# Performance work log

Measured on AMD Instinct MI355X. Metric: run time of the kernel, lower is better.

## Reference

```python
import jax, jax.numpy as jnp
import numpy as np
from jax import lax

VOCAB, EMB, FILT, ATT, KW = 50000, 300, 400, 200, 3
B, N = 4096, 30

def setup_inputs() -> dict:
    key = jax.random.key(0)
    ks = jax.random.split(key, 7)
    encoded_title = jax.random.randint(ks[0], (B, N), 0, VOCAB)
    emb = jax.random.normal(ks[1], (VOCAB, EMB), dtype=jnp.float32) * 0.1
    conv_w = jax.random.normal(ks[2], (FILT, EMB, KW), dtype=jnp.float32) * (1.0 / np.sqrt(EMB * KW))
    conv_b = jnp.zeros((FILT,), dtype=jnp.float32)
    v = jax.random.normal(ks[3], (FILT, ATT), dtype=jnp.float32) * (1.0 / np.sqrt(FILT))
    vb = jnp.zeros((ATT,), dtype=jnp.float32)
    q = jax.random.normal(ks[4], (ATT, 1), dtype=jnp.float32) * (1.0 / np.sqrt(ATT))
    return {"encoded_title": encoded_title, "emb": emb, "conv_w": conv_w,
            "conv_b": conv_b, "v": v, "vb": vb, "q": q}

def reference(encoded_title, emb, conv_w, conv_b, v, vb, q):
    mask = (encoded_title != 0).astype(jnp.float32)          # [B, N]
    W = emb[encoded_title]                                    # [B, N, E]
    x = jnp.transpose(W, (0, 2, 1))                           # [B, E, N]
    C = lax.conv_general_dilated(x, conv_w, window_strides=(1,),
                                 padding=[(1, 1)],
                                 dimension_numbers=("NCH", "OIH", "NCH"))
    C = jnp.transpose(C, (0, 2, 1)) + conv_b                  # [B, N, F]
    C = jax.nn.relu(C)
    a = jnp.tanh(C @ v + vb)                                  # [B, N, A]
    a = (a @ q)[..., 0]                                       # [B, N]
    alpha = jax.nn.softmax(a, axis=0)                         # softmax over batch dim (faithful to dim=0)
    alpha = alpha * mask
    e = jnp.einsum("bn,bnf->bf", alpha, C)                    # batched weighted-sum pooling
    return e
```

## Files before the change

### kernel.cpp

```cpp
#include <hip/hip_runtime.h>
#include <hip/hip_bf16.h>

#define VOCAB 50000
#define EMB   300
#define FILT  400
#define ATT   200
#define BB    4096
#define NN    30

#define ATTP  208
#define KC    416

typedef short bf16x8 __attribute__((ext_vector_type(8)));
typedef float f32x4  __attribute__((ext_vector_type(4)));
typedef unsigned short u16x4 __attribute__((ext_vector_type(4)));

static __device__ __forceinline__ unsigned short f2bf(float f) {
    __hip_bfloat16 h = __float2bfloat16(f);
    union { __hip_bfloat16 h; unsigned short u; } c; c.h = h; return c.u;
}
static __device__ __forceinline__ float bf2f(unsigned short u) {
    union { unsigned int u; float f; } c; c.u = ((unsigned int)u) << 16; return c.f;
}
static __device__ __forceinline__ float fast_tanh(float x) {
    float e = __expf(2.f * x);
    return 1.f - 2.f * __builtin_amdgcn_rcpf(e + 1.f);
}

static __device__ __forceinline__ void dma16(const unsigned short* g, unsigned short* l) {
    __builtin_amdgcn_global_load_lds(
        (const __attribute__((address_space(1))) unsigned int*)(const void*)g,
        (__attribute__((address_space(3))) unsigned int*)(void*)l,
        16, 0, 0);
}

__global__ __launch_bounds__(256) void kP(const float* __restrict__ conv_w,
                                          const float* __restrict__ v,
                                          const float* __restrict__ vb,
                                          const float* __restrict__ q,
                                          unsigned short* __restrict__ Bc2,
                                          unsigned short* __restrict__ Bv2,
                                          float* __restrict__ vbp,
                                          float* __restrict__ qp) {
    int t = blockIdx.x * 256 + threadIdx.x;
    const int NBC = 750 * 512;
    if (t < NBC) {
        int tau = t >> 9, off = t & 511;
        int l = off >> 3, j = off & 7;
        int lm = l & 15, qq = l >> 4;
        int ft = tau % 25, es = (tau / 25) % 10, k = tau / 250;
        int f = ft * 16 + lm;
        int e = es * 32 + qq * 8 + j;
        float val = (e < EMB) ? conv_w[((size_t)f * EMB + e) * 3 + k] : 0.f;
        Bc2[t] = f2bf(val);
    } else {
        int t2 = t - NBC;
        if (t2 < 169 * 512) {
            int tau = t2 >> 9, off = t2 & 511;
            int l = off >> 3, j = off & 7;
            int lm = l & 15, qq = l >> 4;
            int ks = tau / 13, at = tau % 13;
            int att = at * 16 + lm;
            int fcol = ks * 32 + qq * 8 + j;
            float val = (att < ATT && fcol < FILT) ? v[(size_t)fcol * ATT + att] : 0.f;
            Bv2[t2] = f2bf(val);
        }
    }
    if (t < ATTP) {
        vbp[t] = (t < ATT) ? vb[t] : 0.f;
        qp[t]  = (t < ATT) ? q[t] : 0.f;
    }
}

static __device__ __forceinline__ void gatherA(const float* __restrict__ emb,
                                               int tok, int e, float* aR) {
#pragma unroll
    for (int jj = 0; jj < 8; jj++) aR[jj] = 0.f;
    if (tok >= 0 && e < EMB) {
        if (e <= 292) {
            float4 x = *(const float4*)(emb + (size_t)tok * EMB + e);
            float4 y = *(const float4*)(emb + (size_t)tok * EMB + e + 4);
            aR[0] = x.x; aR[1] = x.y; aR[2] = x.z; aR[3] = x.w;
            aR[4] = y.x; aR[5] = y.y; aR[6] = y.z; aR[7] = y.w;
        } else {
#pragma unroll
            for (int jj = 0; jj < 8; jj++) {
                int ee = e + jj;
                if (ee < EMB) aR[jj] = emb[(size_t)tok * EMB + ee];
            }
        }
    }
}

__global__ __launch_bounds__(640, 2) void k1_conv(
    const int* __restrict__ idx,
    const float* __restrict__ emb,
    const unsigned short* __restrict__ Bc2,
    const float* __restrict__ conv_b,
    unsigned short* __restrict__ Cws)
{
    __shared__ unsigned short As[131 * 40];
    __shared__ unsigned short Bs[2 * 25 * 512];
    const int bid = blockIdx.x;
    const int t = threadIdx.x;
    const int lane = t & 63, wave = t >> 6;
    const int lm = lane & 15, qq = lane >> 4;
    const int wg = wave / 5, fw = wave % 5;
    const int rbase = wg * 64;

    const int uj = t >> 2, useg = t & 3;
    const bool uact = (t < 524);
    int utok = -1;
    if (uact && uj < 128) {
        int ub = uj >> 5, uj2 = uj & 31;
        if (uj2 >= 1 && uj2 <= 30) utok = idx[(bid * 4 + ub) * NN + (uj2 - 1)];
    }

    if (wg == 0) {
#pragma unroll
        for (int s = 0; s < 2; s++) {
#pragma unroll
            for (int nt = 0; nt < 5; nt++) {
                int gt = (s % 3) * 250 + (s / 3) * 25 + fw * 5 + nt;
                dma16(Bc2 + (size_t)gt * 512 + lane * 8,
                      Bs + s * 12800 + (fw * 5 + nt) * 512);
            }
        }
    }
    float aR[8];
    gatherA(emb, utok, useg * 8, aR);

    f32x4 acc[4][5];
#pragma unroll
    for (int mt = 0; mt < 4; mt++)
#pragma unroll
        for (int nt = 0; nt < 5; nt++)
            acc[mt][nt] = (f32x4){0.f, 0.f, 0.f, 0.f};

    for (int es = 0; es < 10; ++es) {
        if (uact) {
            union { bf16x8 v; unsigned short u[8]; } cv;
#pragma unroll
            for (int jj = 0; jj < 8; jj++) cv.u[jj] = f2bf(aR[jj]);
            *(bf16x8*)(As + uj * 40 + useg * 8) = cv.v;
        }
        __syncthreads();
        if (es < 9) gatherA(emb, utok, (es + 1) * 32 + useg * 8, aR);

#pragma unroll
        for (int k = 0; k < 3; ++k) {
            const int s = es * 3 + k;
            const unsigned short* bb = Bs + (s & 1) * 12800;
            bf16x8 aF[4];
#pragma unroll
            for (int mt = 0; mt < 4; mt++)
                aF[mt] = *(const bf16x8*)(As + (rbase + mt * 16 + lm + k) * 40 + qq * 8);
#pragma unroll
            for (int nt = 0; nt < 5; nt++) {
                bf16x8 bF = *(const bf16x8*)(bb + (fw * 5 + nt) * 512 + lane * 8);
#pragma unroll
                for (int mt = 0; mt < 4; mt++)
                    acc[mt][nt] = __builtin_amdgcn_mfma_f32_16x16x32_bf16(aF[mt], bF, acc[mt][nt], 0, 0, 0);
            }
            __syncthreads();
            if (s + 2 < 30 && wg == 0) {
                const int s2 = s + 2, es2 = s2 / 3, k2 = s2 - es2 * 3;
#pragma unroll
                for (int nt = 0; nt < 5; nt++) {
                    int gt = (k2 * 10 + es2) * 25 + fw * 5 + nt;
                    dma16(Bc2 + (size_t)gt * 512 + lane * 8,
                          Bs + (s & 1) * 12800 + (fw * 5 + nt) * 512);
                }
            }
        }
    }

    const int f0 = fw * 80;
    float cb[5];
#pragma unroll
    for (int nt = 0; nt < 5; nt++) cb[nt] = conv_b[f0 + nt * 16 + lm];
#pragma unroll
    for (int mt = 0; mt < 4; mt++) {
#pragma unroll
        for (int r = 0; r < 4; r++) {
            int lrow = rbase + mt * 16 + qq * 4 + r;
            int n = lrow & 31;
            int bglob = bid * 4 + (lrow >> 5);
            if (n < NN) {
#pragma unroll
                for (int nt = 0; nt < 5; nt++) {
                    float vv = fmaxf(acc[mt][nt][r] + cb[nt], 0.f);
                    Cws[((size_t)bglob * NN + n) * FILT + f0 + nt * 16 + lm] = f2bf(vv);
                }
            }
        }
    }
}

__global__ __launch_bounds__(256, 2) void k2_att(
    const unsigned short* __restrict__ Cws,
    const unsigned short* __restrict__ Bv2,
    const float* __restrict__ vbp, const float* __restrict__ qp,
    float* __restrict__ a_out)
{
    __shared__ unsigned short Bs[2 * 13 * 512];
    const int lane = threadIdx.x & 63;
    const int wave = threadIdx.x >> 6;
    const int lm = lane & 15, qq = lane >> 4;
    const int r0 = blockIdx.x * 128 + wave * 32;

#pragma unroll
    for (int s = 0; s < 2; s++)
#pragma unroll
        for (int nt = 0; nt < 13; nt++)
            if ((nt & 3) == wave)
                dma16(Bv2 + (size_t)(s * 13 + nt) * 512 + lane * 8,
                      Bs + s * 6656 + nt * 512);

    bf16x8 aFc[2], aFn[2];
#pragma unroll
    for (int mt = 0; mt < 2; mt++)
        aFc[mt] = *(const bf16x8*)(Cws + (size_t)(r0 + mt * 16 + lm) * FILT + 8 * qq);

    f32x4 acc[2][13];
#pragma unroll
    for (int mt = 0; mt < 2; mt++)
#pragma unroll
        for (int nt = 0; nt < 13; nt++) acc[mt][nt] = (f32x4){0.f, 0.f, 0.f, 0.f};

    __syncthreads();

    for (int ks = 0; ks < 13; ++ks) {
        if (ks < 12)
#pragma unroll
            for (int mt = 0; mt < 2; mt++)
                aFn[mt] = *(const bf16x8*)(Cws + (size_t)(r0 + mt * 16 + lm) * FILT + (ks + 1) * 32 + 8 * qq);
        const unsigned short* bb = Bs + (ks & 1) * 6656;
#pragma unroll
        for (int nt = 0; nt < 13; nt++) {
            bf16x8 bF = *(const bf16x8*)(bb + nt * 512 + lane * 8);
#pragma unroll
            for (int mt = 0; mt < 2; mt++)
                acc[mt][nt] = __builtin_amdgcn_mfma_f32_16x16x32_bf16(aFc[mt], bF, acc[mt][nt], 0, 0, 0);
        }
        __syncthreads();
        if (ks + 2 < 13)
#pragma unroll
            for (int nt = 0; nt < 13; nt++)
                if ((nt & 3) == wave)
                    dma16(Bv2 + (size_t)((ks + 2) * 13 + nt) * 512 + lane * 8,
                          Bs + (ks & 1) * 6656 + nt * 512);
#pragma unroll
        for (int mt = 0; mt < 2; mt++) aFc[mt] = aFn[mt];
    }

#pragma unroll
    for (int mt = 0; mt < 2; mt++) {
        float rs[4] = {0.f, 0.f, 0.f, 0.f};
#pragma unroll
        for (int nt = 0; nt < 13; nt++) {
            int att = nt * 16 + lm;
            float vbv = vbp[att], qv = qp[att];
#pragma unroll
            for (int r = 0; r < 4; r++)
                rs[r] += fast_tanh(acc[mt][nt][r] + vbv) * qv;
        }
#pragma unroll
        for (int off = 1; off < 16; off <<= 1)
#pragma unroll
            for (int r = 0; r < 4; r++) rs[r] += __shfl_xor(rs[r], off, 64);
        if (lm == 0) {
#pragma unroll
            for (int r = 0; r < 4; r++) a_out[r0 + mt * 16 + qq * 4 + r] = rs[r];
        }
    }
}

__global__ __launch_bounds__(256) void k3_softmax(float* __restrict__ a,
                                                  const int* __restrict__ idx) {
    int n = blockIdx.x;
    int tid = threadIdx.x;
    constexpr int PER = BB / 256;
    float vals[PER];
    float m = -1e30f;
#pragma unroll
    for (int i = 0; i < PER; i++) {
        int b = i * 256 + tid;
        vals[i] = a[b * NN + n];
        m = fmaxf(m, vals[i]);
    }
    __shared__ float red[8];
#pragma unroll
    for (int off = 32; off >= 1; off >>= 1) m = fmaxf(m, __shfl_xor(m, off, 64));
    int wave = tid >> 6;
    if ((tid & 63) == 0) red[wave] = m;
    __syncthreads();
    m = fmaxf(fmaxf(red[0], red[1]), fmaxf(red[2], red[3]));

    float s = 0.f;
#pragma unroll
    for (int i = 0; i < PER; i++) {
        vals[i] = expf(vals[i] - m);
        s += vals[i];
    }
#pragma unroll
    for (int off = 32; off >= 1; off >>= 1) s += __shfl_xor(s, off, 64);
    if ((tid & 63) == 0) red[4 + wave] = s;
    __syncthreads();
    s = red[4] + red[5] + red[6] + red[7];
    float inv = 1.f / s;
#pragma unroll
    for (int i = 0; i < PER; i++) {
        int b = i * 256 + tid;
        float msk = (idx[b * NN + n] != 0) ? 1.f : 0.f;
        a[b * NN + n] = vals[i] * inv * msk;
    }
}

__global__ __launch_bounds__(128) void k4_pool(
    const float* __restrict__ alpha, const unsigned short* __restrict__ C,
    float* __restrict__ out)
{
    int b = blockIdx.x;
    int tid = threadIdx.x;
    __shared__ float al[NN];
    if (tid < NN) al[tid] = alpha[b * NN + tid];
    __syncthreads();
    if (tid < 100) {
        int f = tid * 4;
        float s0 = 0.f, s1 = 0.f, s2 = 0.f, s3 = 0.f;
        const unsigned short* Cb = C + (size_t)b * (NN * FILT) + f;
#pragma unroll
        for (int n = 0; n < NN; n++) {
            u16x4 c = *(const u16x4*)(Cb + (size_t)n * FILT);
            float a = al[n];
            s0 = fmaf(a, bf2f(c[0]), s0);
            s1 = fmaf(a, bf2f(c[1]), s1);
            s2 = fmaf(a, bf2f(c[2]), s2);
            s3 = fmaf(a, bf2f(c[3]), s3);
        }
        float4 o; o.x = s0; o.y = s1; o.z = s2; o.w = s3;
        *(float4*)(out + (size_t)b * FILT + f) = o;
    }
}

extern "C" void kernel_launch(void* const* d_in, const int* in_sizes, int n_in,
                              void* d_out, int out_size, void* d_ws, size_t ws_size,
                              hipStream_t stream) {
    const int*   idx    = (const int*)d_in[0];
    const float* emb    = (const float*)d_in[1];
    const float* conv_w = (const float*)d_in[2];
    const float* conv_b = (const float*)d_in[3];
    const float* v      = (const float*)d_in[4];
    const float* vb     = (const float*)d_in[5];
    const float* q      = (const float*)d_in[6];
    float* out = (float*)d_out;

    char* ws = (char*)d_ws;
    size_t o = 0;
    unsigned short* Bv2 = (unsigned short*)(ws + o); o += (size_t)169 * 512 * 2;
    float* vbp = (float*)(ws + o);                   o += 1024;
    float* qp  = (float*)(ws + o);                   o += 1024;
    unsigned short* Bc2 = (unsigned short*)(ws + o);
    float* a_buf = (float*)(ws + o);
    o += (size_t)750 * 512 * 2;
    unsigned short* Cws = (unsigned short*)(ws + o);

    const int NP = 750 * 512 + 169 * 512;
    kP<<<(NP + 255) / 256, 256, 0, stream>>>(conv_w, v, vb, q, Bc2, Bv2, vbp, qp);
    k1_conv<<<BB / 4, 640, 0, stream>>>(idx, emb, Bc2, conv_b, Cws);
    k2_att<<<(BB * NN) / 128, 256, 0, stream>>>(Cws, Bv2, vbp, qp, a_buf);
    k3_softmax<<<NN, 256, 0, stream>>>(a_buf, idx);
    k4_pool<<<BB, 128, 0, stream>>>(a_buf, Cws, out);
}
```

Measured before the change: 282.0 us.

## Fuse attention projection into conv kernel via LDS-staged C tiles

The attention GEMM, tanh and q-dot are moved into the conv kernel's epilogue. Each block stages its bf16 C tile in shared memory (unioned with the matmul buffers) and computes attention scores there with MFMA, reading V directly from global memory. This removes the separate k2 launch and its re-read of C from global memory. Scores are written transposed ([N][B]) into the output buffer as scratch, so softmax reads them coalesced with 1024-thread blocks and float4 loads. In exchange the conv kernel gets more syncs, more LDS pressure and uncached B-operand loads in the fused stage.

```diff
diff --git a/kernel.cpp b/kernel.cpp
--- a/kernel.cpp
+++ b/kernel.cpp
@@ -9,7 +9,7 @@
 #define NN    30
 
 #define ATTP  208
-#define KC    416
+#define CLS   424
 
 typedef short bf16x8 __attribute__((ext_vector_type(8)));
 typedef float f32x4  __attribute__((ext_vector_type(4)));
@@ -97,10 +97,19 @@
     const float* __restrict__ emb,
     const unsigned short* __restrict__ Bc2,
     const float* __restrict__ conv_b,
-    unsigned short* __restrict__ Cws)
+    const unsigned short* __restrict__ Bv2,
+    const float* __restrict__ vbp,
+    const float* __restrict__ qp,
+    unsigned short* __restrict__ Cws,
+    float* __restrict__ aG)
 {
-    __shared__ unsigned short As[131 * 40];
-    __shared__ unsigned short Bs[2 * 25 * 512];
+    __shared__ union {
+        struct { unsigned short As[131 * 40]; unsigned short Bs[2 * 25 * 512]; } mm;
+        struct { unsigned short Cl[64 * CLS]; float wp[160]; } at;
+    } sh;
+    unsigned short* const As = sh.mm.As;
+    unsigned short* const Bs = sh.mm.Bs;
+
     const int bid = blockIdx.x;
     const int t = threadIdx.x;
     const int lane = t & 63, wave = t >> 6;
@@ -179,142 +188,114 @@
     float cb[5];
 #pragma unroll
     for (int nt = 0; nt < 5; nt++) cb[nt] = conv_b[f0 + nt * 16 + lm];
-#pragma unroll
-    for (int mt = 0; mt < 4; mt++) {
-#pragma unroll
-        for (int r = 0; r < 4; r++) {
-            int lrow = rbase + mt * 16 + qq * 4 + r;
-            int n = lrow & 31;
-            int bglob = bid * 4 + (lrow >> 5);
-            if (n < NN) {
-#pragma unroll
-                for (int nt = 0; nt < 5; nt++) {
-                    float vv = fmaxf(acc[mt][nt][r] + cb[nt], 0.f);
-                    Cws[((size_t)bglob * NN + n) * FILT + f0 + nt * 16 + lm] = f2bf(vv);
+
+    const int rt = wave & 3;
+    const int widx = wave >> 2;
+    const int nW = (rt < 2) ? 3 : 2;
+
+#pragma unroll
+    for (int h = 0; h < 2; ++h) {
+        if (wg == h) {
+#pragma unroll
+            for (int mt = 0; mt < 4; mt++) {
+#pragma unroll
+                for (int r = 0; r < 4; r++) {
+                    int lr = mt * 16 + qq * 4 + r;
+                    int lrow = h * 64 + lr;
+                    int pos = lrow & 31, grp = lrow >> 5;
+#pragma unroll
+                    for (int nt = 0; nt < 5; nt++) {
+                        float vv = fmaxf(acc[mt][nt][r] + cb[nt], 0.f);
+                        unsigned short bv = f2bf(vv);
+                        sh.at.Cl[lr * CLS + f0 + nt * 16 + lm] = bv;
+                        if (pos < NN)
+                            Cws[((size_t)(bid * 4 + grp) * NN + pos) * FILT + f0 + nt * 16 + lm] = bv;
+                    }
                 }
             }
         }
-    }
-}
-
-__global__ __launch_bounds__(256, 2) void k2_att(
-    const unsigned short* __restrict__ Cws,
-    const unsigned short* __restrict__ Bv2,
-    const float* __restrict__ vbp, const float* __restrict__ qp,
-    float* __restrict__ a_out)
-{
-    __shared__ unsigned short Bs[2 * 13 * 512];
-    const int lane = threadIdx.x & 63;
-    const int wave = threadIdx.x >> 6;
-    const int lm = lane & 15, qq = lane >> 4;
-    const int r0 = blockIdx.x * 128 + wave * 32;
-
-#pragma unroll
-    for (int s = 0; s < 2; s++)
-#pragma unroll
-        for (int nt = 0; nt < 13; nt++)
-            if ((nt & 3) == wave)
-                dma16(Bv2 + (size_t)(s * 13 + nt) * 512 + lane * 8,
-                      Bs + s * 6656 + nt * 512);
-
-    bf16x8 aFc[2], aFn[2];
-#pragma unroll
-    for (int mt = 0; mt < 2; mt++)
-        aFc[mt] = *(const bf16x8*)(Cws + (size_t)(r0 + mt * 16 + lm) * FILT + 8 * qq);
-
-    f32x4 acc[2][13];
-#pragma unroll
-    for (int mt = 0; mt < 2; mt++)
-#pragma unroll
-        for (int nt = 0; nt < 13; nt++) acc[mt][nt] = (f32x4){0.f, 0.f, 0.f, 0.f};
-
+        if (h == 0) {
+            for (int i = t; i < 64 * 16; i += 640)
+                sh.at.Cl[(i >> 4) * CLS + 400 + (i & 15)] = 0;
+        }
+        __syncthreads();
+
+        float rs0 = 0.f, rs1 = 0.f, rs2 = 0.f, rs3 = 0.f;
+        for (int ct = widx; ct < 13; ct += nW) {
+            f32x4 sA = (f32x4){0.f, 0.f, 0.f, 0.f};
+            f32x4 sB = (f32x4){0.f, 0.f, 0.f, 0.f};
+#pragma unroll
+            for (int ks = 0; ks < 13; ks++) {
+                bf16x8 aF = *(const bf16x8*)(sh.at.Cl + (rt * 16 + lm) * CLS + ks * 32 + qq * 8);
+                bf16x8 bF = *(const bf16x8*)(Bv2 + (size_t)(ks * 13 + ct) * 512 + lane * 8);
+                if (ks & 1) sB = __builtin_amdgcn_mfma_f32_16x16x32_bf16(aF, bF, sB, 0, 0, 0);
+                else        sA = __builtin_amdgcn_mfma_f32_16x16x32_bf16(aF, bF, sA, 0, 0, 0);
+            }
+            int att = ct * 16 + lm;
+            float vbv = vbp[att], qv = qp[att];
+            float p0 = fast_tanh(sA[0] + sB[0] + vbv) * qv;
+            float p1 = fast_tanh(sA[1] + sB[1] + vbv) * qv;
+            float p2 = fast_tanh(sA[2] + sB[2] + vbv) * qv;
+            float p3 = fast_tanh(sA[3] + sB[3] + vbv) * qv;
+#pragma unroll
+            for (int off = 1; off < 16; off <<= 1) {
+                p0 += __shfl_xor(p0, off, 64);
+                p1 += __shfl_xor(p1, off, 64);
+                p2 += __shfl_xor(p2, off, 64);
+                p3 += __shfl_xor(p3, off, 64);
+            }
+            if (lm == 0) { rs0 += p0; rs1 += p1; rs2 += p2; rs3 += p3; }
+        }
+        if (lm == 0) {
+            sh.at.wp[wave * 16 + qq * 4 + 0] = rs0;
+            sh.at.wp[wave * 16 + qq * 4 + 1] = rs1;
+            sh.at.wp[wave * 16 + qq * 4 + 2] = rs2;
+            sh.at.wp[wave * 16 + qq * 4 + 3] = rs3;
+        }
+        __syncthreads();
+        if (t < 64) {
+            int rr = t >> 4, ii = t & 15;
+            float sum = 0.f;
+            for (int w = rr; w < 10; w += 4) sum += sh.at.wp[w * 16 + ii];
+            int lrow = h * 64 + t;
+            int pos = lrow & 31, grp = lrow >> 5;
+            if (pos < NN) aG[(size_t)pos * BB + bid * 4 + grp] = sum;
+        }
+    }
+}
+
+__global__ __launch_bounds__(1024) void k3_softmax(const float* __restrict__ a,
+                                                   float* __restrict__ alpha,
+                                                   const int* __restrict__ idx) {
+    int n = blockIdx.x, tid = threadIdx.x;
+    float4 v4 = *(const float4*)(a + (size_t)n * BB + tid * 4);
+    float m = fmaxf(fmaxf(v4.x, v4.y), fmaxf(v4.z, v4.w));
+    __shared__ float red[32];
+#pragma unroll
+    for (int off = 32; off >= 1; off >>= 1) m = fmaxf(m, __shfl_xor(m, off, 64));
+    int wv = tid >> 6;
+    if ((tid & 63) == 0) red[wv] = m;
     __syncthreads();
-
-    for (int ks = 0; ks < 13; ++ks) {
-        if (ks < 12)
-#pragma unroll
-            for (int mt = 0; mt < 2; mt++)
-                aFn[mt] = *(const bf16x8*)(Cws + (size_t)(r0 + mt * 16 + lm) * FILT + (ks + 1) * 32 + 8 * qq);
-        const unsigned short* bb = Bs + (ks & 1) * 6656;
-#pragma unroll
-        for (int nt = 0; nt < 13; nt++) {
-            bf16x8 bF = *(const bf16x8*)(bb + nt * 512 + lane * 8);
-#pragma unroll
-            for (int mt = 0; mt < 2; mt++)
-                acc[mt][nt] = __builtin_amdgcn_mfma_f32_16x16x32_bf16(aFc[mt], bF, acc[mt][nt], 0, 0, 0);
-        }
-        __syncthreads();
-        if (ks + 2 < 13)
-#pragma unroll
-            for (int nt = 0; nt < 13; nt++)
-                if ((nt & 3) == wave)
-                    dma16(Bv2 + (size_t)((ks + 2) * 13 + nt) * 512 + lane * 8,
-                          Bs + (ks & 1) * 6656 + nt * 512);
-#pragma unroll
-        for (int mt = 0; mt < 2; mt++) aFc[mt] = aFn[mt];
-    }
-
-#pragma unroll
-    for (int mt = 0; mt < 2; mt++) {
-        float rs[4] = {0.f, 0.f, 0.f, 0.f};
-#pragma unroll
-        for (int nt = 0; nt < 13; nt++) {
-            int att = nt * 16 + lm;
-            float vbv = vbp[att], qv = qp[att];
-#pragma unroll
-            for (int r = 0; r < 4; r++)
-                rs[r] += fast_tanh(acc[mt][nt][r] + vbv) * qv;
-        }
-#pragma unroll
-        for (int off = 1; off < 16; off <<= 1)
-#pragma unroll
-            for (int r = 0; r < 4; r++) rs[r] += __shfl_xor(rs[r], off, 64);
-        if (lm == 0) {
-#pragma unroll
-            for (int r = 0; r < 4; r++) a_out[r0 + mt * 16 + qq * 4 + r] = rs[r];
-        }
-    }
-}
-
-__global__ __launch_bounds__(256) void k3_softmax(float* __restrict__ a,
-                                                  const int* __restrict__ idx) {
-    int n = blockIdx.x;
-    int tid = threadIdx.x;
-    constexpr int PER = BB / 256;
-    float vals[PER];
-    float m = -1e30f;
-#pragma unroll
-    for (int i = 0; i < PER; i++) {
-        int b = i * 256 + tid;
-        vals[i] = a[b * NN + n];
-        m = fmaxf(m, vals[i]);
-    }
-    __shared__ float red[8];
-#pragma unroll
-    for (int off = 32; off >= 1; off >>= 1) m = fmaxf(m, __shfl_xor(m, off, 64));
-    int wave = tid >> 6;
-    if ((tid & 63) == 0) red[wave] = m;
+#pragma unroll
+    for (int w = 0; w < 16; w++) m = fmaxf(m, red[w]);
+    float e0 = expf(v4.x - m), e1 = expf(v4.y - m);
+    float e2 = expf(v4.z - m), e3 = expf(v4.w - m);
+    float s = e0 + e1 + e2 + e3;
+#pragma unroll
+    for (int off = 32; off >= 1; off >>= 1) s += __shfl_xor(s, off, 64);
+    if ((tid & 63) == 0) red[16 + wv] = s;
     __syncthreads();
-    m = fmaxf(fmaxf(red[0], red[1]), fmaxf(red[2], red[3]));
-
-    float s = 0.f;
-#pragma unroll
-    for (int i = 0; i < PER; i++) {
-        vals[i] = expf(vals[i] - m);
-        s += vals[i];
-    }
-#pragma unroll
-    for (int off = 32; off >= 1; off >>= 1) s += __shfl_xor(s, off, 64);
-    if ((tid & 63) == 0) red[4 + wave] = s;
-    __syncthreads();
-    s = red[4] + red[5] + red[6] + red[7];
+    s = 0.f;
+#pragma unroll
+    for (int w = 0; w < 16; w++) s += red[16 + w];
     float inv = 1.f / s;
-#pragma unroll
-    for (int i = 0; i < PER; i++) {
-        int b = i * 256 + tid;
-        float msk = (idx[b * NN + n] != 0) ? 1.f : 0.f;
-        a[b * NN + n] = vals[i] * inv * msk;
-    }
+    int b0 = tid * 4;
+    float4 o;
+    o.x = e0 * inv * ((idx[(size_t)(b0 + 0) * NN + n] != 0) ? 1.f : 0.f);
+    o.y = e1 * inv * ((idx[(size_t)(b0 + 1) * NN + n] != 0) ? 1.f : 0.f);
+    o.z = e2 * inv * ((idx[(size_t)(b0 + 2) * NN + n] != 0) ? 1.f : 0.f);
+    o.w = e3 * inv * ((idx[(size_t)(b0 + 3) * NN + n] != 0) ? 1.f : 0.f);
+    *(float4*)(alpha + (size_t)n * BB + b0) = o;
 }
 
 __global__ __launch_bounds__(128) void k4_pool(
@@ -324,7 +305,7 @@
     int b = blockIdx.x;
     int tid = threadIdx.x;
     __shared__ float al[NN];
-    if (tid < NN) al[tid] = alpha[b * NN + tid];
+    if (tid < NN) al[tid] = alpha[(size_t)tid * BB + b];
     __syncthreads();
     if (tid < 100) {
         int f = tid * 4;
@@ -362,14 +343,15 @@
     float* vbp = (float*)(ws + o);                   o += 1024;
     float* qp  = (float*)(ws + o);                   o += 1024;
     unsigned short* Bc2 = (unsigned short*)(ws + o);
-    float* a_buf = (float*)(ws + o);
+    float* alpha = (float*)(ws + o);
     o += (size_t)750 * 512 * 2;
     unsigned short* Cws = (unsigned short*)(ws + o);
 
+    float* aG = out;
+
     const int NP = 750 * 512 + 169 * 512;
     kP<<<(NP + 255) / 256, 256, 0, stream>>>(conv_w, v, vb, q, Bc2, Bv2, vbp, qp);
-    k1_conv<<<BB / 4, 640, 0, stream>>>(idx, emb, Bc2, conv_b, Cws);
-    k2_att<<<(BB * NN) / 128, 256, 0, stream>>>(Cws, Bv2, vbp, qp, a_buf);
-    k3_softmax<<<NN, 256, 0, stream>>>(a_buf, idx);
-    k4_pool<<<BB, 128, 0, stream>>>(a_buf, Cws, out);
-}
+    k1_conv<<<BB / 4, 640, 0, stream>>>(idx, emb, Bc2, conv_b, Bv2, vbp, qp, Cws, aG);
+    k3_softmax<<<NN, 1024, 0, stream>>>(aG, alpha, idx);
+    k4_pool<<<BB, 128, 0, stream>>>(alpha, Cws, out);
+}
```

After: 366.1 us. +29.8%, slower.
